# Performance work log

Measured on AMD Instinct MI355X. Metric: run time of the kernel, lower is better.

The kernel has to match this reference:

```python
import jax, jax.numpy as jnp
import numpy as np

D = 256        # node/edge feature dim
H = 256        # MLP hidden dim
NG = 80000     # grid (src) nodes
NM = 20000     # mesh (dst) nodes
E = 160000     # g2m edges
EPS = 1e-5


def _mlp(x, W1, b1, W2, b2, g, beta):
    # MeshGraphMLP with hidden_layers=1: Linear -> SiLU -> Linear -> LayerNorm
    h = jax.nn.silu(x @ W1 + b1)
    y = h @ W2 + b2
    mu = jnp.mean(y, axis=-1, keepdims=True)
    var = jnp.var(y, axis=-1, keepdims=True)
    return (y - mu) * jax.lax.rsqrt(var + EPS) * g + beta


def setup_inputs() -> dict:
    key = jax.random.key(0)
    ks = jax.random.split(key, 16)

    def rn(k, shape, s=0.02):
        return jax.random.normal(k, shape, dtype=jnp.float32) * s

    inp = {
        "g2m_efeat": jax.random.normal(ks[0], (E, D), dtype=jnp.float32),
        "grid_nfeat": jax.random.normal(ks[1], (NG, D), dtype=jnp.float32),
        "mesh_nfeat": jax.random.normal(ks[2], (NM, D), dtype=jnp.float32),
        "src_idx": jax.random.randint(ks[3], (E,), 0, NG, dtype=jnp.int32),
        "dst_idx": jax.random.randint(ks[4], (E,), 0, NM, dtype=jnp.int32),
        # edge MLP (concat variant): input = [efeat | src_feat | dst_feat] -> 3D
        "eW1": rn(ks[5], (3 * D, H)), "eb1": jnp.zeros((H,), jnp.float32),
        "eW2": rn(ks[6], (H, D)),     "eb2": jnp.zeros((D,), jnp.float32),
        "eg": jnp.ones((D,), jnp.float32), "ebeta": jnp.zeros((D,), jnp.float32),
        # src node MLP: D -> H -> D
        "sW1": rn(ks[7], (D, H)), "sb1": jnp.zeros((H,), jnp.float32),
        "sW2": rn(ks[8], (H, D)), "sb2": jnp.zeros((D,), jnp.float32),
        "sg": jnp.ones((D,), jnp.float32), "sbeta": jnp.zeros((D,), jnp.float32),
        # dst node MLP: (D_agg + D_node) = 2D -> H -> D
        "dW1": rn(ks[9], (2 * D, H)), "db1": jnp.zeros((H,), jnp.float32),
        "dW2": rn(ks[10], (H, D)),    "db2": jnp.zeros((D,), jnp.float32),
        "dg": jnp.ones((D,), jnp.float32), "dbeta": jnp.zeros((D,), jnp.float32),
    }
    return inp


def reference(g2m_efeat, grid_nfeat, mesh_nfeat, src_idx, dst_idx,
              eW1, eb1, eW2, eb2, eg, ebeta,
              sW1, sb1, sW2, sb2, sg, sbeta,
              dW1, db1, dW2, db2, dg, dbeta):
    # edge MLP: gather src/dst node features, concat with edge features
    e_in = jnp.concatenate(
        [g2m_efeat, grid_nfeat[src_idx], mesh_nfeat[dst_idx]], axis=-1)  # [E, 3D]
    efeat = _mlp(e_in, eW1, eb1, eW2, eb2, eg, ebeta)                    # [E, D]
    # aggregate_and_concat: copy_e_sum scatter to dst mesh nodes, concat node feats
    agg = jax.ops.segment_sum(efeat, dst_idx, num_segments=NM)           # [NM, D]
    cat_feat = jnp.concatenate([agg, mesh_nfeat], axis=-1)               # [NM, 2D]
    mesh_out = mesh_nfeat + _mlp(cat_feat, dW1, db1, dW2, db2, dg, dbeta)
    grid_out = grid_nfeat + _mlp(grid_nfeat, sW1, sb1, sW2, sb2, sg, sbeta)
    return (grid_out, mesh_out)
```

## Files before the change

kernel.cpp:

```cpp
#include <hip/hip_runtime.h>
#include <hip/hip_bf16.h>

#define DD 256
#define NGN 80000
#define NMN 20000
#define NEE 160000

typedef unsigned short u16;
typedef __attribute__((ext_vector_type(8))) short s16x8;
typedef __attribute__((ext_vector_type(4))) short s16x4;
typedef __attribute__((ext_vector_type(4))) float f32x4;

__device__ __forceinline__ u16 f2bf(float f) {
  union { float f; unsigned u; } v; v.f = f;
  unsigned r = (v.u + 0x7FFFu + ((v.u >> 16) & 1u)) >> 16;
  return (u16)r;
}
__device__ __forceinline__ float bf2f(u16 x) {
  union { unsigned u; float f; } v; v.u = ((unsigned)x) << 16;
  return v.f;
}

__global__ void pack_weights(const float* __restrict__ W, u16* __restrict__ dst, int K) {
  int idx = blockIdx.x * 256 + threadIdx.x;
  if (idx >= K * 256) return;
  int i = idx & 7;
  int lane = (idx >> 3) & 63;
  int nt = (idx >> 9) & 15;
  int kt = idx >> 13;
  int k = kt * 32 + 4 * (lane >> 4) + (i < 4 ? i : 12 + i);
  int n = nt * 16 + (lane & 15);
  dst[idx] = f2bf(W[(size_t)k * 256 + n]);
}

__global__ void csr_hist(const int* __restrict__ didx, int* __restrict__ cnt) {
  int i = blockIdx.x * 256 + threadIdx.x;
  if (i < NEE) atomicAdd(cnt + didx[i], 1);
}
__global__ void csr_scan(const int* __restrict__ cnt, int* __restrict__ cursor) {
  __shared__ int psum[256];
  const int CH = (NMN + 255) / 256;
  int t = threadIdx.x;
  int base = t * CH, s = 0;
  for (int k = 0; k < CH; ++k) { int i = base + k; if (i < NMN) s += cnt[i]; }
  psum[t] = s;
  __syncthreads();
  for (int off = 1; off < 256; off <<= 1) {
    int v = (t >= off) ? psum[t - off] : 0;
    __syncthreads();
    psum[t] += v;
    __syncthreads();
  }
  int run = psum[t] - s;
  for (int k = 0; k < CH; ++k) {
    int i = base + k;
    if (i < NMN) { cursor[i] = run; run += cnt[i]; }
  }
}
__global__ void csr_fill(const int* __restrict__ didx, int* __restrict__ cursor,
                         int* __restrict__ eids) {
  int e = blockIdx.x * 256 + threadIdx.x;
  if (e < NEE) { int p = atomicAdd(cursor + didx[e], 1); eids[p] = e; }
}

__device__ __forceinline__ s16x8 ldsA(const u16* uni, int rowL, int cL) {
  int swz = (rowL & 7) << 4;
  s16x4 lo = *(const s16x4*)((const char*)uni + rowL * 512 + ((cL * 2) ^ swz));
  s16x4 hi = *(const s16x4*)((const char*)uni + rowL * 512 + (((cL + 16) * 2) ^ swz));
  s16x8 a;
#pragma unroll
  for (int j = 0; j < 4; ++j) { a[j] = lo[j]; a[4 + j] = hi[j]; }
  return a;
}

__global__ __launch_bounds__(256, 2) void gemm_ns(
    const float* __restrict__ X, const u16* __restrict__ Wp,
    u16* __restrict__ Y, int n) {
  __shared__ u16 uni[16384];
  const int tid = threadIdx.x;
  const int lane = tid & 63;
  const int wave = tid >> 6;
  const int mr = wave >> 1, nc = wave & 1;
  const int g = lane >> 4, lr = lane & 15;
  const int row0 = blockIdx.x * 64;

#pragma unroll
  for (int j = 0; j < 8; ++j) {
    int e = wave * 16 + j * 2 + (lane >> 5);
    int r = min(row0 + e, n - 1);
    const float* src = X + (size_t)r * DD + (lane & 31) * 8;
    f32x4 f0 = *(const f32x4*)src;
    f32x4 f1 = *(const f32x4*)(src + 4);
    s16x8 o;
#pragma unroll
    for (int k = 0; k < 4; ++k) { o[k] = (short)f2bf(f0[k]); o[4 + k] = (short)f2bf(f1[k]); }
    int co = (lane & 31) * 8;
    *(s16x8*)((char*)uni + e * 512 + ((co * 2) ^ ((e & 7) << 4))) = o;
  }
  __syncthreads();

  const f32x4 fz = {0.f, 0.f, 0.f, 0.f};
  f32x4 acc[2][8];
#pragma unroll
  for (int mt = 0; mt < 2; ++mt)
#pragma unroll
    for (int nt = 0; nt < 8; ++nt) acc[mt][nt] = fz;

  for (int kl = 0; kl < 8; ++kl) {
    s16x8 afr[2];
#pragma unroll
    for (int mt = 0; mt < 2; ++mt) afr[mt] = ldsA(uni, mr * 32 + mt * 16 + lr, kl * 32 + 4 * g);
#pragma unroll
    for (int h = 0; h < 2; ++h) {
      s16x8 bfr[4];
#pragma unroll
      for (int q = 0; q < 4; ++q)
        bfr[q] = *(const s16x8*)(Wp + (size_t)kl * 8192 + ((nc * 8 + h * 4 + q) * 64 + lane) * 8);
#pragma unroll
      for (int q = 0; q < 4; ++q) {
        acc[0][h * 4 + q] = __builtin_amdgcn_mfma_f32_16x16x32_bf16(afr[0], bfr[q], acc[0][h * 4 + q], 0, 0, 0);
        acc[1][h * 4 + q] = __builtin_amdgcn_mfma_f32_16x16x32_bf16(afr[1], bfr[q], acc[1][h * 4 + q], 0, 0, 0);
      }
    }
  }
  __syncthreads();
#pragma unroll
  for (int mt = 0; mt < 2; ++mt)
#pragma unroll
    for (int nt = 0; nt < 8; ++nt)
#pragma unroll
      for (int i = 0; i < 4; ++i) {
        int rowL = mr * 32 + mt * 16 + 4 * g + i;
        int col = nc * 128 + nt * 16 + lr;
        *(u16*)((char*)uni + rowL * 512 + ((col * 2) ^ ((rowL & 7) << 4))) = f2bf(acc[mt][nt][i]);
      }
  __syncthreads();
#pragma unroll
  for (int rr = 0; rr < 16; ++rr) {
    int rowL = wave * 16 + rr;
    int rg = row0 + rowL;
    if (rg < n) {
      s16x4 v = *(const s16x4*)((char*)uni + rowL * 512 + ((lane * 8) ^ ((rowL & 7) << 4)));
      *(s16x4*)(Y + (size_t)rg * DD + lane * 4) = v;
    }
  }
}

__global__ __launch_bounds__(256, 2) void edge_fused(
    const float* __restrict__ efeat,
    const u16* __restrict__ GSp, const u16* __restrict__ GMp,
    const int* __restrict__ sidx, const int* __restrict__ eids,
    const u16* __restrict__ W1p, const float* __restrict__ b1,
    const u16* __restrict__ W2p, const float* __restrict__ b2,
    const float* __restrict__ gam, const float* __restrict__ bet,
    const int* __restrict__ didx, float* __restrict__ agg) {
  __shared__ u16 uni[16384];
  __shared__ float2 pstats[64][2];
  __shared__ int eidL[64];
  __shared__ int srcL[64];
  __shared__ int dstL[64];

  const int tid = threadIdx.x;
  const int lane = tid & 63;
  const int wave = tid >> 6;
  const int mr = wave >> 1, nc = wave & 1;
  const int g = lane >> 4, lr = lane & 15;
  const int row0 = blockIdx.x * 64;

  if (tid < 64) {
    int e = eids[row0 + tid];
    eidL[tid] = e;
    srcL[tid] = sidx[e];
    dstL[tid] = didx[e];
  }
  __syncthreads();

#pragma unroll
  for (int j = 0; j < 8; ++j) {
    int e = wave * 16 + j * 2 + (lane >> 5);
    int co = (lane & 31) * 8;
    s16x8 a = *(const s16x8*)(GSp + (size_t)srcL[e] * DD + co);
    s16x8 b = *(const s16x8*)(GMp + (size_t)dstL[e] * DD + co);
    s16x8 o;
#pragma unroll
    for (int k = 0; k < 8; ++k) o[k] = (short)f2bf(bf2f((u16)a[k]) + bf2f((u16)b[k]));
    *(s16x8*)((char*)uni + e * 512 + ((co * 2) ^ ((e & 7) << 4))) = o;
  }
  __syncthreads();

  f32x4 acc[2][8];
#pragma unroll
  for (int mt = 0; mt < 2; ++mt)
#pragma unroll
    for (int nt = 0; nt < 8; ++nt)
#pragma unroll
      for (int i = 0; i < 4; ++i) {
        int rowL = mr * 32 + mt * 16 + 4 * g + i;
        int col = nc * 128 + nt * 16 + lr;
        acc[mt][nt][i] = bf2f(*(const u16*)((char*)uni + rowL * 512 + ((col * 2) ^ ((rowL & 7) << 4))));
      }
  __syncthreads();

#pragma unroll
  for (int j = 0; j < 8; ++j) {
    int e = wave * 16 + j * 2 + (lane >> 5);
    const float* src = efeat + (size_t)eidL[e] * DD + (lane & 31) * 8;
    f32x4 f0 = *(const f32x4*)src;
    f32x4 f1 = *(const f32x4*)(src + 4);
    s16x8 o;
#pragma unroll
    for (int k = 0; k < 4; ++k) { o[k] = (short)f2bf(f0[k]); o[4 + k] = (short)f2bf(f1[k]); }
    int co = (lane & 31) * 8;
    *(s16x8*)((char*)uni + e * 512 + ((co * 2) ^ ((e & 7) << 4))) = o;
  }
  __syncthreads();

  for (int kl = 0; kl < 8; ++kl) {
    s16x8 afr[2];
#pragma unroll
    for (int mt = 0; mt < 2; ++mt) afr[mt] = ldsA(uni, mr * 32 + mt * 16 + lr, kl * 32 + 4 * g);
#pragma unroll
    for (int h = 0; h < 2; ++h) {
      s16x8 bfr[4];
#pragma unroll
      for (int q = 0; q < 4; ++q)
        bfr[q] = *(const s16x8*)(W1p + (size_t)kl * 8192 + ((nc * 8 + h * 4 + q) * 64 + lane) * 8);
#pragma unroll
      for (int q = 0; q < 4; ++q) {
        acc[0][h * 4 + q] = __builtin_amdgcn_mfma_f32_16x16x32_bf16(afr[0], bfr[q], acc[0][h * 4 + q], 0, 0, 0);
        acc[1][h * 4 + q] = __builtin_amdgcn_mfma_f32_16x16x32_bf16(afr[1], bfr[q], acc[1][h * 4 + q], 0, 0, 0);
      }
    }
  }
  __syncthreads();

  {
    float b1v[8];
#pragma unroll
    for (int nt = 0; nt < 8; ++nt) b1v[nt] = b1[nc * 128 + nt * 16 + lr];
#pragma unroll
    for (int mt = 0; mt < 2; ++mt)
#pragma unroll
      for (int nt = 0; nt < 8; ++nt)
#pragma unroll
        for (int i = 0; i < 4; ++i) {
          float x = acc[mt][nt][i] + b1v[nt];
          float h = x / (1.f + __expf(-x));
          int rowL = mr * 32 + mt * 16 + 4 * g + i;
          int col = nc * 128 + nt * 16 + lr;
          *(u16*)((char*)uni + rowL * 512 + ((col * 2) ^ ((rowL & 7) << 4))) = f2bf(h);
        }
  }
  __syncthreads();

  f32x4 acc2[2][8];
  const f32x4 fz = {0.f, 0.f, 0.f, 0.f};
#pragma unroll
  for (int mt = 0; mt < 2; ++mt)
#pragma unroll
    for (int nt = 0; nt < 8; ++nt) acc2[mt][nt] = fz;
  for (int kl = 0; kl < 8; ++kl) {
    s16x8 afr[2];
#pragma unroll
    for (int mt = 0; mt < 2; ++mt) afr[mt] = ldsA(uni, mr * 32 + mt * 16 + lr, kl * 32 + 4 * g);
#pragma unroll
    for (int h = 0; h < 2; ++h) {
      s16x8 bfr[4];
#pragma unroll
      for (int q = 0; q < 4; ++q)
        bfr[q] = *(const s16x8*)(W2p + (size_t)kl * 8192 + ((nc * 8 + h * 4 + q) * 64 + lane) * 8);
#pragma unroll
      for (int q = 0; q < 4; ++q) {
        acc2[0][h * 4 + q] = __builtin_amdgcn_mfma_f32_16x16x32_bf16(afr[0], bfr[q], acc2[0][h * 4 + q], 0, 0, 0);
        acc2[1][h * 4 + q] = __builtin_amdgcn_mfma_f32_16x16x32_bf16(afr[1], bfr[q], acc2[1][h * 4 + q], 0, 0, 0);
      }
    }
  }

  float b2v[8], gv[8], bv[8];
#pragma unroll
  for (int nt = 0; nt < 8; ++nt) {
    int col = nc * 128 + nt * 16 + lr;
    b2v[nt] = b2[col];
    gv[nt] = gam[col];
    bv[nt] = bet[col];
  }
#pragma unroll
  for (int mt = 0; mt < 2; ++mt)
#pragma unroll
    for (int i = 0; i < 4; ++i) {
      float s = 0.f, s2 = 0.f;
#pragma unroll
      for (int nt = 0; nt < 8; ++nt) {
        float y = acc2[mt][nt][i] + b2v[nt];
        s += y;
        s2 += y * y;
      }
#pragma unroll
      for (int m = 1; m < 16; m <<= 1) {
        s += __shfl_xor(s, m);
        s2 += __shfl_xor(s2, m);
      }
      if (lr == 0) pstats[mr * 32 + mt * 16 + 4 * g + i][nc] = make_float2(s, s2);
    }
  __syncthreads();

#pragma unroll
  for (int mt = 0; mt < 2; ++mt)
#pragma unroll
    for (int i = 0; i < 4; ++i) {
      int rowL = mr * 32 + mt * 16 + 4 * g + i;
      float2 pa = pstats[rowL][0], pb = pstats[rowL][1];
      float sum = pa.x + pb.x, sq = pa.y + pb.y;
      float mu = sum * (1.f / 256.f);
      float var = fmaxf(sq * (1.f / 256.f) - mu * mu, 0.f);
      float rs = rsqrtf(var + 1e-5f);
#pragma unroll
      for (int nt = 0; nt < 8; ++nt) {
        int col = nc * 128 + nt * 16 + lr;
        float y = acc2[mt][nt][i] + b2v[nt];
        float val = (y - mu) * rs * gv[nt] + bv[nt];
        *(u16*)((char*)uni + rowL * 512 + ((col * 2) ^ ((rowL & 7) << 4))) = f2bf(val);
      }
    }
  __syncthreads();

  {
    int c = tid;
    float sum = 0.f;
    int prev = dstL[0];
#pragma unroll 8
    for (int r = 0; r < 64; ++r) {
      int d = dstL[r];
      if (d != prev) {
        atomicAdd(agg + (size_t)prev * DD + c, sum);
        sum = 0.f;
        prev = d;
      }
      sum += bf2f(*(const u16*)((char*)uni + r * 512 + ((c * 2) ^ ((r & 7) << 4))));
    }
    atomicAdd(agg + (size_t)prev * DD + c, sum);
  }
}

template <int MODE, int K1>
__global__ __launch_bounds__(256, 2) void mlp_fused(
    const float* __restrict__ xa, const float* __restrict__ xb,
    const u16* __restrict__ W1p, const float* __restrict__ b1,
    const u16* __restrict__ W2p, const float* __restrict__ b2,
    const float* __restrict__ gam, const float* __restrict__ bet,
    const float* __restrict__ resid, float* __restrict__ out, int nrows) {
  __shared__ u16 uni[16384];
  __shared__ float2 pstats[64][2];

  const int tid = threadIdx.x;
  const int lane = tid & 63;
  const int wave = tid >> 6;
  const int mr = wave >> 1, nc = wave & 1;
  const int g = lane >> 4, lr = lane & 15;
  const int row0 = blockIdx.x * 64;

  const f32x4 fz = {0.f, 0.f, 0.f, 0.f};
  f32x4 acc[2][8];
#pragma unroll
  for (int mt = 0; mt < 2; ++mt)
#pragma unroll
    for (int nt = 0; nt < 8; ++nt) acc[mt][nt] = fz;

#pragma unroll
  for (int region = 0; region < K1 / 256; ++region) {
    __syncthreads();
    const float* Xr = (region == 0) ? xa : xb;
#pragma unroll
    for (int j = 0; j < 8; ++j) {
      int e = wave * 16 + j * 2 + (lane >> 5);
      int r = min(row0 + e, nrows - 1);
      const float* src = Xr + (size_t)r * DD + (lane & 31) * 8;
      f32x4 f0 = *(const f32x4*)src;
      f32x4 f1 = *(const f32x4*)(src + 4);
      s16x8 o;
#pragma unroll
      for (int k = 0; k < 4; ++k) { o[k] = (short)f2bf(f0[k]); o[4 + k] = (short)f2bf(f1[k]); }
      int co = (lane & 31) * 8;
      *(s16x8*)((char*)uni + e * 512 + ((co * 2) ^ ((e & 7) << 4))) = o;
    }
    __syncthreads();
    for (int kl = 0; kl < 8; ++kl) {
      const int kt = region * 8 + kl;
      s16x8 afr[2];
#pragma unroll
      for (int mt = 0; mt < 2; ++mt) afr[mt] = ldsA(uni, mr * 32 + mt * 16 + lr, kl * 32 + 4 * g);
#pragma unroll
      for (int h = 0; h < 2; ++h) {
        s16x8 bfr[4];
#pragma unroll
        for (int q = 0; q < 4; ++q)
          bfr[q] = *(const s16x8*)(W1p + (size_t)kt * 8192 + ((nc * 8 + h * 4 + q) * 64 + lane) * 8);
#pragma unroll
        for (int q = 0; q < 4; ++q) {
          acc[0][h * 4 + q] = __builtin_amdgcn_mfma_f32_16x16x32_bf16(afr[0], bfr[q], acc[0][h * 4 + q], 0, 0, 0);
          acc[1][h * 4 + q] = __builtin_amdgcn_mfma_f32_16x16x32_bf16(afr[1], bfr[q], acc[1][h * 4 + q], 0, 0, 0);
        }
      }
    }
  }
  __syncthreads();

  {
    float b1v[8];
#pragma unroll
    for (int nt = 0; nt < 8; ++nt) b1v[nt] = b1[nc * 128 + nt * 16 + lr];
#pragma unroll
    for (int mt = 0; mt < 2; ++mt)
#pragma unroll
      for (int nt = 0; nt < 8; ++nt)
#pragma unroll
        for (int i = 0; i < 4; ++i) {
          float x = acc[mt][nt][i] + b1v[nt];
          float h = x / (1.f + __expf(-x));
          int rowL = mr * 32 + mt * 16 + 4 * g + i;
          int col = nc * 128 + nt * 16 + lr;
          *(u16*)((char*)uni + rowL * 512 + ((col * 2) ^ ((rowL & 7) << 4))) = f2bf(h);
        }
  }
  __syncthreads();

  f32x4 acc2[2][8];
#pragma unroll
  for (int mt = 0; mt < 2; ++mt)
#pragma unroll
    for (int nt = 0; nt < 8; ++nt) acc2[mt][nt] = fz;
  for (int kl = 0; kl < 8; ++kl) {
    s16x8 afr[2];
#pragma unroll
    for (int mt = 0; mt < 2; ++mt) afr[mt] = ldsA(uni, mr * 32 + mt * 16 + lr, kl * 32 + 4 * g);
#pragma unroll
    for (int h = 0; h < 2; ++h) {
      s16x8 bfr[4];
#pragma unroll
      for (int q = 0; q < 4; ++q)
        bfr[q] = *(const s16x8*)(W2p + (size_t)kl * 8192 + ((nc * 8 + h * 4 + q) * 64 + lane) * 8);
#pragma unroll
      for (int q = 0; q < 4; ++q) {
        acc2[0][h * 4 + q] = __builtin_amdgcn_mfma_f32_16x16x32_bf16(afr[0], bfr[q], acc2[0][h * 4 + q], 0, 0, 0);
        acc2[1][h * 4 + q] = __builtin_amdgcn_mfma_f32_16x16x32_bf16(afr[1], bfr[q], acc2[1][h * 4 + q], 0, 0, 0);
      }
    }
  }

  float b2v[8], gv[8], bv[8];
#pragma unroll
  for (int nt = 0; nt < 8; ++nt) {
    int col = nc * 128 + nt * 16 + lr;
    b2v[nt] = b2[col];
    gv[nt] = gam[col];
    bv[nt] = bet[col];
  }
#pragma unroll
  for (int mt = 0; mt < 2; ++mt)
#pragma unroll
    for (int i = 0; i < 4; ++i) {
      float s = 0.f, s2 = 0.f;
#pragma unroll
      for (int nt = 0; nt < 8; ++nt) {
        float y = acc2[mt][nt][i] + b2v[nt];
        s += y;
        s2 += y * y;
      }
#pragma unroll
      for (int m = 1; m < 16; m <<= 1) {
        s += __shfl_xor(s, m);
        s2 += __shfl_xor(s2, m);
      }
      if (lr == 0) pstats[mr * 32 + mt * 16 + 4 * g + i][nc] = make_float2(s, s2);
    }
  __syncthreads();
#pragma unroll
  for (int mt = 0; mt < 2; ++mt)
#pragma unroll
    for (int i = 0; i < 4; ++i) {
      int rowL = mr * 32 + mt * 16 + 4 * g + i;
      float2 pa = pstats[rowL][0], pb = pstats[rowL][1];
      float sum = pa.x + pb.x, sq = pa.y + pb.y;
      float mu = sum * (1.f / 256.f);
      float var = fmaxf(sq * (1.f / 256.f) - mu * mu, 0.f);
      float rs = rsqrtf(var + 1e-5f);
      int rg = row0 + rowL;
      if (MODE == 2 && rg >= nrows) continue;
#pragma unroll
      for (int nt = 0; nt < 8; ++nt) {
        int col = nc * 128 + nt * 16 + lr;
        float y = acc2[mt][nt][i] + b2v[nt];
        float val = (y - mu) * rs * gv[nt] + bv[nt];
        out[(size_t)rg * DD + col] = resid[(size_t)rg * DD + col] + val;
      }
    }
}

extern "C" void kernel_launch(void* const* d_in, const int* in_sizes, int n_in,
                              void* d_out, int out_size, void* d_ws, size_t ws_size,
                              hipStream_t stream) {
  const float* g2m  = (const float*)d_in[0];
  const float* grid = (const float*)d_in[1];
  const float* mesh = (const float*)d_in[2];
  const int* sidx = (const int*)d_in[3];
  const int* didx = (const int*)d_in[4];
  const float* eW1 = (const float*)d_in[5];
  const float* eb1 = (const float*)d_in[6];
  const float* eW2 = (const float*)d_in[7];
  const float* eb2 = (const float*)d_in[8];
  const float* eg  = (const float*)d_in[9];
  const float* ebt = (const float*)d_in[10];
  const float* sW1 = (const float*)d_in[11];
  const float* sb1 = (const float*)d_in[12];
  const float* sW2 = (const float*)d_in[13];
  const float* sb2 = (const float*)d_in[14];
  const float* sg  = (const float*)d_in[15];
  const float* sbt = (const float*)d_in[16];
  const float* dW1 = (const float*)d_in[17];
  const float* db1 = (const float*)d_in[18];
  const float* dW2 = (const float*)d_in[19];
  const float* db2 = (const float*)d_in[20];
  const float* dg  = (const float*)d_in[21];
  const float* dbt = (const float*)d_in[22];

  char* w = (char*)d_ws;
  float* agg = (float*)w;
  u16* wp = (u16*)(w + 20480000);
  int* cnt = (int*)(w + 20480000 + 1179648);
  int* cursor = cnt + 20480;
  int* eids = cursor + 20480;

  u16* eW1p = wp;
  u16* eW2p = eW1p + 768 * 256;
  u16* sW1p = eW2p + 256 * 256;
  u16* sW2p = sW1p + 256 * 256;
  u16* dW1p = sW2p + 256 * 256;
  u16* dW2p = dW1p + 512 * 256;

  float* gout = (float*)d_out;
  float* mout = gout + (size_t)NGN * DD;
  u16* GSp = (u16*)d_out;
  u16* GMp = GSp + (size_t)NGN * DD;

  (void)hipMemsetAsync(agg, 0, 20480000, stream);
  (void)hipMemsetAsync(cnt, 0, 81920, stream);

  pack_weights<<<768, 256, 0, stream>>>(eW1, eW1p, 768);
  pack_weights<<<256, 256, 0, stream>>>(eW2, eW2p, 256);
  pack_weights<<<256, 256, 0, stream>>>(sW1, sW1p, 256);
  pack_weights<<<256, 256, 0, stream>>>(sW2, sW2p, 256);
  pack_weights<<<512, 256, 0, stream>>>(dW1, dW1p, 512);
  pack_weights<<<256, 256, 0, stream>>>(dW2, dW2p, 256);

  csr_hist<<<(NEE + 255) / 256, 256, 0, stream>>>(didx, cnt);
  csr_scan<<<1, 256, 0, stream>>>(cnt, cursor);
  csr_fill<<<(NEE + 255) / 256, 256, 0, stream>>>(didx, cursor, eids);

  gemm_ns<<<NGN / 64, 256, 0, stream>>>(grid, eW1p + 8 * 8192, GSp, NGN);
  gemm_ns<<<(NMN + 63) / 64, 256, 0, stream>>>(mesh, eW1p + 16 * 8192, GMp, NMN);

  edge_fused<<<NEE / 64, 256, 0, stream>>>(
      g2m, GSp, GMp, sidx, eids, eW1p, eb1, eW2p, eb2, eg, ebt, didx, agg);

  mlp_fused<2, 512><<<(NMN + 63) / 64, 256, 0, stream>>>(
      agg, mesh, dW1p, db1, dW2p, db2, dg, dbt, mesh, mout, NMN);
  mlp_fused<1, 256><<<NGN / 64, 256, 0, stream>>>(
      grid, nullptr, sW1p, sb1, sW2p, sb2, sg, sbt, grid, gout, NGN);
}
```

Baseline: 426.0 us.

## Merge small launches and co-schedule grid MLP blocks with edge MLP blocks

Folds the six weight-pack launches and the CSR histogram into one kernel, and merges the projection GEMMs with the CSR fill into another. When workspace allows, the projected node features move out of the output buffer so the grid-node MLP can run interleaved with edge blocks (every third block) in one launch, removing the serial dependency. The goal is fewer launches and better overlap of independent work. The cost is larger kernels whose branch-dependent register and shared-memory use may lower occupancy. Rounding now goes through the library bf16 conversion.

```diff
diff --git a/kernel.cpp b/kernel.cpp
--- a/kernel.cpp
+++ b/kernel.cpp
@@ -12,31 +12,50 @@
 typedef __attribute__((ext_vector_type(4))) float f32x4;
 
 __device__ __forceinline__ u16 f2bf(float f) {
-  union { float f; unsigned u; } v; v.f = f;
-  unsigned r = (v.u + 0x7FFFu + ((v.u >> 16) & 1u)) >> 16;
-  return (u16)r;
+  __hip_bfloat16 h = __float2bfloat16(f);
+  union { __hip_bfloat16 h; u16 u; } v; v.h = h;
+  return v.u;
 }
 __device__ __forceinline__ float bf2f(u16 x) {
   union { unsigned u; float f; } v; v.u = ((unsigned)x) << 16;
   return v.f;
 }
 
-__global__ void pack_weights(const float* __restrict__ W, u16* __restrict__ dst, int K) {
-  int idx = blockIdx.x * 256 + threadIdx.x;
-  if (idx >= K * 256) return;
-  int i = idx & 7;
-  int lane = (idx >> 3) & 63;
-  int nt = (idx >> 9) & 15;
-  int kt = idx >> 13;
-  int k = kt * 32 + 4 * (lane >> 4) + (i < 4 ? i : 12 + i);
-  int n = nt * 16 + (lane & 15);
-  dst[idx] = f2bf(W[(size_t)k * 256 + n]);
-}
-
-__global__ void csr_hist(const int* __restrict__ didx, int* __restrict__ cnt) {
-  int i = blockIdx.x * 256 + threadIdx.x;
-  if (i < NEE) atomicAdd(cnt + didx[i], 1);
-}
+__device__ __forceinline__ s16x8 ldsA(const u16* uni, int rowL, int cL) {
+  int swz = (rowL & 7) << 4;
+  s16x4 lo = *(const s16x4*)((const char*)uni + rowL * 512 + ((cL * 2) ^ swz));
+  s16x4 hi = *(const s16x4*)((const char*)uni + rowL * 512 + (((cL + 16) * 2) ^ swz));
+  s16x8 a;
+#pragma unroll
+  for (int j = 0; j < 4; ++j) { a[j] = lo[j]; a[4 + j] = hi[j]; }
+  return a;
+}
+
+__global__ void pack_hist(const float* __restrict__ eW1, const float* __restrict__ eW2,
+                          const float* __restrict__ sW1, const float* __restrict__ sW2,
+                          const float* __restrict__ dW1, const float* __restrict__ dW2,
+                          u16* __restrict__ wp, const int* __restrict__ didx,
+                          int* __restrict__ cnt) {
+  int bid = blockIdx.x;
+  if (bid < 2304) {
+    const float* W; u16* dst; int lb;
+    if (bid < 768)       { W = eW1; dst = wp;              lb = bid; }
+    else if (bid < 1024) { W = eW2; dst = wp + 768 * 256;  lb = bid - 768; }
+    else if (bid < 1280) { W = sW1; dst = wp + 1024 * 256; lb = bid - 1024; }
+    else if (bid < 1536) { W = sW2; dst = wp + 1280 * 256; lb = bid - 1280; }
+    else if (bid < 2048) { W = dW1; dst = wp + 1536 * 256; lb = bid - 1536; }
+    else                 { W = dW2; dst = wp + 2048 * 256; lb = bid - 2048; }
+    int idx = lb * 256 + threadIdx.x;
+    int i = idx & 7, lane = (idx >> 3) & 63, nt = (idx >> 9) & 15, kt = idx >> 13;
+    int k = kt * 32 + 4 * (lane >> 4) + (i < 4 ? i : 12 + i);
+    int n = nt * 16 + (lane & 15);
+    dst[idx] = f2bf(W[(size_t)k * 256 + n]);
+  } else {
+    int i = (bid - 2304) * 256 + threadIdx.x;
+    if (i < NEE) atomicAdd(cnt + didx[i], 1);
+  }
+}
+
 __global__ void csr_scan(const int* __restrict__ cnt, int* __restrict__ cursor) {
   __shared__ int psum[256];
   const int CH = (NMN + 255) / 256;
@@ -57,32 +76,16 @@
     if (i < NMN) { cursor[i] = run; run += cnt[i]; }
   }
 }
-__global__ void csr_fill(const int* __restrict__ didx, int* __restrict__ cursor,
-                         int* __restrict__ eids) {
-  int e = blockIdx.x * 256 + threadIdx.x;
-  if (e < NEE) { int p = atomicAdd(cursor + didx[e], 1); eids[p] = e; }
-}
-
-__device__ __forceinline__ s16x8 ldsA(const u16* uni, int rowL, int cL) {
-  int swz = (rowL & 7) << 4;
-  s16x4 lo = *(const s16x4*)((const char*)uni + rowL * 512 + ((cL * 2) ^ swz));
-  s16x4 hi = *(const s16x4*)((const char*)uni + rowL * 512 + (((cL + 16) * 2) ^ swz));
-  s16x8 a;
-#pragma unroll
-  for (int j = 0; j < 4; ++j) { a[j] = lo[j]; a[4 + j] = hi[j]; }
-  return a;
-}
-
-__global__ __launch_bounds__(256, 2) void gemm_ns(
-    const float* __restrict__ X, const u16* __restrict__ Wp,
-    u16* __restrict__ Y, int n) {
-  __shared__ u16 uni[16384];
+
+__device__ __forceinline__ void gemm_body(u16* uni, const float* __restrict__ X,
+                                          const u16* __restrict__ Wp, u16* __restrict__ Y,
+                                          int n, int blk) {
   const int tid = threadIdx.x;
   const int lane = tid & 63;
   const int wave = tid >> 6;
   const int mr = wave >> 1, nc = wave & 1;
   const int g = lane >> 4, lr = lane & 15;
-  const int row0 = blockIdx.x * 64;
+  const int row0 = blk * 64;
 
 #pragma unroll
   for (int j = 0; j < 8; ++j) {
@@ -146,26 +149,187 @@
   }
 }
 
-__global__ __launch_bounds__(256, 2) void edge_fused(
+__global__ __launch_bounds__(256, 2) void gemm_fill(
+    const float* __restrict__ gridf, const float* __restrict__ mesh,
+    const u16* __restrict__ wp, u16* __restrict__ GSp, u16* __restrict__ GMp,
+    const int* __restrict__ didx, int* __restrict__ cursor, int* __restrict__ eids) {
+  __shared__ u16 uni[16384];
+  int bid = blockIdx.x;
+  if (bid < 1250) gemm_body(uni, gridf, wp + 8 * 8192, GSp, NGN, bid);
+  else if (bid < 1563) gemm_body(uni, mesh, wp + 16 * 8192, GMp, NMN, bid - 1250);
+  else {
+    int e = (bid - 1563) * 256 + threadIdx.x;
+    if (e < NEE) { int p = atomicAdd(cursor + didx[e], 1); eids[p] = e; }
+  }
+}
+
+template <int MODE, int K1>
+__device__ __forceinline__ void mlp_body(
+    u16* uni, float2 (*pstats)[2],
+    const float* __restrict__ xa, const float* __restrict__ xb,
+    const u16* __restrict__ W1p, const float* __restrict__ b1,
+    const u16* __restrict__ W2p, const float* __restrict__ b2,
+    const float* __restrict__ gam, const float* __restrict__ bet,
+    const float* __restrict__ resid, float* __restrict__ out, int nrows, int blk) {
+  const int tid = threadIdx.x;
+  const int lane = tid & 63;
+  const int wave = tid >> 6;
+  const int mr = wave >> 1, nc = wave & 1;
+  const int g = lane >> 4, lr = lane & 15;
+  const int row0 = blk * 64;
+
+  const f32x4 fz = {0.f, 0.f, 0.f, 0.f};
+  f32x4 acc[2][8];
+#pragma unroll
+  for (int mt = 0; mt < 2; ++mt)
+#pragma unroll
+    for (int nt = 0; nt < 8; ++nt) acc[mt][nt] = fz;
+
+#pragma unroll
+  for (int region = 0; region < K1 / 256; ++region) {
+    __syncthreads();
+    const float* Xr = (region == 0) ? xa : xb;
+#pragma unroll
+    for (int j = 0; j < 8; ++j) {
+      int e = wave * 16 + j * 2 + (lane >> 5);
+      int r = min(row0 + e, nrows - 1);
+      const float* src = Xr + (size_t)r * DD + (lane & 31) * 8;
+      f32x4 f0 = *(const f32x4*)src;
+      f32x4 f1 = *(const f32x4*)(src + 4);
+      s16x8 o;
+#pragma unroll
+      for (int k = 0; k < 4; ++k) { o[k] = (short)f2bf(f0[k]); o[4 + k] = (short)f2bf(f1[k]); }
+      int co = (lane & 31) * 8;
+      *(s16x8*)((char*)uni + e * 512 + ((co * 2) ^ ((e & 7) << 4))) = o;
+    }
+    __syncthreads();
+    for (int kl = 0; kl < 8; ++kl) {
+      const int kt = region * 8 + kl;
+      s16x8 afr[2];
+#pragma unroll
+      for (int mt = 0; mt < 2; ++mt) afr[mt] = ldsA(uni, mr * 32 + mt * 16 + lr, kl * 32 + 4 * g);
+#pragma unroll
+      for (int h = 0; h < 2; ++h) {
+        s16x8 bfr[4];
+#pragma unroll
+        for (int q = 0; q < 4; ++q)
+          bfr[q] = *(const s16x8*)(W1p + (size_t)kt * 8192 + ((nc * 8 + h * 4 + q) * 64 + lane) * 8);
+#pragma unroll
+        for (int q = 0; q < 4; ++q) {
+          acc[0][h * 4 + q] = __builtin_amdgcn_mfma_f32_16x16x32_bf16(afr[0], bfr[q], acc[0][h * 4 + q], 0, 0, 0);
+          acc[1][h * 4 + q] = __builtin_amdgcn_mfma_f32_16x16x32_bf16(afr[1], bfr[q], acc[1][h * 4 + q], 0, 0, 0);
+        }
+      }
+    }
+  }
+  __syncthreads();
+
+  {
+    float b1v[8];
+#pragma unroll
+    for (int nt = 0; nt < 8; ++nt) b1v[nt] = b1[nc * 128 + nt * 16 + lr];
+#pragma unroll
+    for (int mt = 0; mt < 2; ++mt)
+#pragma unroll
+      for (int nt = 0; nt < 8; ++nt)
+#pragma unroll
+        for (int i = 0; i < 4; ++i) {
+          float x = acc[mt][nt][i] + b1v[nt];
+          float h = x / (1.f + __expf(-x));
+          int rowL = mr * 32 + mt * 16 + 4 * g + i;
+          int col = nc * 128 + nt * 16 + lr;
+          *(u16*)((char*)uni + rowL * 512 + ((col * 2) ^ ((rowL & 7) << 4))) = f2bf(h);
+        }
+  }
+  __syncthreads();
+
+  f32x4 acc2[2][8];
+#pragma unroll
+  for (int mt = 0; mt < 2; ++mt)
+#pragma unroll
+    for (int nt = 0; nt < 8; ++nt) acc2[mt][nt] = fz;
+  for (int kl = 0; kl < 8; ++kl) {
+    s16x8 afr[2];
+#pragma unroll
+    for (int mt = 0; mt < 2; ++mt) afr[mt] = ldsA(uni, mr * 32 + mt * 16 + lr, kl * 32 + 4 * g);
+#pragma unroll
+    for (int h = 0; h < 2; ++h) {
+      s16x8 bfr[4];
+#pragma unroll
+      for (int q = 0; q < 4; ++q)
+        bfr[q] = *(const s16x8*)(W2p + (size_t)kl * 8192 + ((nc * 8 + h * 4 + q) * 64 + lane) * 8);
+#pragma unroll
+      for (int q = 0; q < 4; ++q) {
+        acc2[0][h * 4 + q] = __builtin_amdgcn_mfma_f32_16x16x32_bf16(afr[0], bfr[q], acc2[0][h * 4 + q], 0, 0, 0);
+        acc2[1][h * 4 + q] = __builtin_amdgcn_mfma_f32_16x16x32_bf16(afr[1], bfr[q], acc2[1][h * 4 + q], 0, 0, 0);
+      }
+    }
+  }
+
+  float b2v[8], gv[8], bv[8];
+#pragma unroll
+  for (int nt = 0; nt < 8; ++nt) {
+    int col = nc * 128 + nt * 16 + lr;
+    b2v[nt] = b2[col];
+    gv[nt] = gam[col];
+    bv[nt] = bet[col];
+  }
+#pragma unroll
+  for (int mt = 0; mt < 2; ++mt)
+#pragma unroll
+    for (int i = 0; i < 4; ++i) {
+      float s = 0.f, s2 = 0.f;
+#pragma unroll
+      for (int nt = 0; nt < 8; ++nt) {
+        float y = acc2[mt][nt][i] + b2v[nt];
+        s += y;
+        s2 += y * y;
+      }
+#pragma unroll
+      for (int m = 1; m < 16; m <<= 1) {
+        s += __shfl_xor(s, m);
+        s2 += __shfl_xor(s2, m);
+      }
+      if (lr == 0) pstats[mr * 32 + mt * 16 + 4 * g + i][nc] = make_float2(s, s2);
+    }
+  __syncthreads();
+#pragma unroll
+  for (int mt = 0; mt < 2; ++mt)
+#pragma unroll
+    for (int i = 0; i < 4; ++i) {
+      int rowL = mr * 32 + mt * 16 + 4 * g + i;
+      float2 pa = pstats[rowL][0], pb = pstats[rowL][1];
+      float sum = pa.x + pb.x, sq = pa.y + pb.y;
+      float mu = sum * (1.f / 256.f);
+      float var = fmaxf(sq * (1.f / 256.f) - mu * mu, 0.f);
+      float rs = rsqrtf(var + 1e-5f);
+      int rg = row0 + rowL;
+      if (MODE == 2 && rg >= nrows) continue;
+#pragma unroll
+      for (int nt = 0; nt < 8; ++nt) {
+        int col = nc * 128 + nt * 16 + lr;
+        float y = acc2[mt][nt][i] + b2v[nt];
+        float val = (y - mu) * rs * gv[nt] + bv[nt];
+        out[(size_t)rg * DD + col] = resid[(size_t)rg * DD + col] + val;
+      }
+    }
+}
+
+__device__ __forceinline__ void edge_body(
+    u16* uni, float2 (*pstats)[2], int* eidL, int* srcL, int* dstL,
     const float* __restrict__ efeat,
     const u16* __restrict__ GSp, const u16* __restrict__ GMp,
     const int* __restrict__ sidx, const int* __restrict__ eids,
     const u16* __restrict__ W1p, const float* __restrict__ b1,
     const u16* __restrict__ W2p, const float* __restrict__ b2,
     const float* __restrict__ gam, const float* __restrict__ bet,
-    const int* __restrict__ didx, float* __restrict__ agg) {
-  __shared__ u16 uni[16384];
-  __shared__ float2 pstats[64][2];
-  __shared__ int eidL[64];
-  __shared__ int srcL[64];
-  __shared__ int dstL[64];
-
+    const int* __restrict__ didx, float* __restrict__ agg, int blk) {
   const int tid = threadIdx.x;
   const int lane = tid & 63;
   const int wave = tid >> 6;
   const int mr = wave >> 1, nc = wave & 1;
   const int g = lane >> 4, lr = lane & 15;
-  const int row0 = blockIdx.x * 64;
+  const int row0 = blk * 64;
 
   if (tid < 64) {
     int e = eids[row0 + tid];
@@ -183,7 +347,8 @@
     s16x8 b = *(const s16x8*)(GMp + (size_t)dstL[e] * DD + co);
     s16x8 o;
 #pragma unroll
-    for (int k = 0; k < 8; ++k) o[k] = (short)f2bf(bf2f((u16)a[k]) + bf2f((u16)b[k]));
+    for (int k2 = 0; k2 < 8; ++k2)
+      o[k2] = (short)f2bf(bf2f((u16)a[k2]) + bf2f((u16)b[k2]));
     *(s16x8*)((char*)uni + e * 512 + ((co * 2) ^ ((e & 7) << 4))) = o;
   }
   __syncthreads();
@@ -343,158 +508,57 @@
   }
 }
 
-template <int MODE, int K1>
-__global__ __launch_bounds__(256, 2) void mlp_fused(
-    const float* __restrict__ xa, const float* __restrict__ xb,
+__global__ __launch_bounds__(256, 2) void edge_mlp(
+    const float* __restrict__ efeat,
+    const u16* __restrict__ GSp, const u16* __restrict__ GMp,
+    const int* __restrict__ sidx, const int* __restrict__ eids,
+    const u16* __restrict__ eW1p, const float* __restrict__ eb1,
+    const u16* __restrict__ eW2p, const float* __restrict__ eb2,
+    const float* __restrict__ eg, const float* __restrict__ ebt,
+    const int* __restrict__ didx, float* __restrict__ agg,
+    const float* __restrict__ gridf,
+    const u16* __restrict__ sW1p, const float* __restrict__ sb1,
+    const u16* __restrict__ sW2p, const float* __restrict__ sb2,
+    const float* __restrict__ sg, const float* __restrict__ sbt,
+    float* __restrict__ gout, int withMlp) {
+  __shared__ u16 uni[16384];
+  __shared__ float2 pstats[64][2];
+  __shared__ int eidL[64], srcL[64], dstL[64];
+  int bid = blockIdx.x;
+  if (withMlp) {
+    if ((bid % 3) == 2) {
+      mlp_body<1, 256>(uni, pstats, gridf, nullptr, sW1p, sb1, sW2p, sb2,
+                       sg, sbt, gridf, gout, NGN, bid / 3);
+      return;
+    }
+    bid = (bid / 3) * 2 + (bid % 3);
+  }
+  edge_body(uni, pstats, eidL, srcL, dstL, efeat, GSp, GMp, sidx, eids,
+            eW1p, eb1, eW2p, eb2, eg, ebt, didx, agg, bid);
+}
+
+__global__ __launch_bounds__(256, 2) void mlp1_kernel(
+    const float* __restrict__ gridf,
     const u16* __restrict__ W1p, const float* __restrict__ b1,
     const u16* __restrict__ W2p, const float* __restrict__ b2,
     const float* __restrict__ gam, const float* __restrict__ bet,
-    const float* __restrict__ resid, float* __restrict__ out, int nrows) {
+    float* __restrict__ out) {
   __shared__ u16 uni[16384];
   __shared__ float2 pstats[64][2];
-
-  const int tid = threadIdx.x;
-  const int lane = tid & 63;
-  const int wave = tid >> 6;
-  const int mr = wave >> 1, nc = wave & 1;
-  const int g = lane >> 4, lr = lane & 15;
-  const int row0 = blockIdx.x * 64;
-
-  const f32x4 fz = {0.f, 0.f, 0.f, 0.f};
-  f32x4 acc[2][8];
-#pragma unroll
-  for (int mt = 0; mt < 2; ++mt)
-#pragma unroll
-    for (int nt = 0; nt < 8; ++nt) acc[mt][nt] = fz;
-
-#pragma unroll
-  for (int region = 0; region < K1 / 256; ++region) {
-    __syncthreads();
-    const float* Xr = (region == 0) ? xa : xb;
-#pragma unroll
-    for (int j = 0; j < 8; ++j) {
-      int e = wave * 16 + j * 2 + (lane >> 5);
-      int r = min(row0 + e, nrows - 1);
-      const float* src = Xr + (size_t)r * DD + (lane & 31) * 8;
-      f32x4 f0 = *(const f32x4*)src;
-      f32x4 f1 = *(const f32x4*)(src + 4);
-      s16x8 o;
-#pragma unroll
-      for (int k = 0; k < 4; ++k) { o[k] = (short)f2bf(f0[k]); o[4 + k] = (short)f2bf(f1[k]); }
-      int co = (lane & 31) * 8;
-      *(s16x8*)((char*)uni + e * 512 + ((co * 2) ^ ((e & 7) << 4))) = o;
-    }
-    __syncthreads();
-    for (int kl = 0; kl < 8; ++kl) {
-      const int kt = region * 8 + kl;
-      s16x8 afr[2];
-#pragma unroll
-      for (int mt = 0; mt < 2; ++mt) afr[mt] = ldsA(uni, mr * 32 + mt * 16 + lr, kl * 32 + 4 * g);
-#pragma unroll
-      for (int h = 0; h < 2; ++h) {
-        s16x8 bfr[4];
-#pragma unroll
-        for (int q = 0; q < 4; ++q)
-          bfr[q] = *(const s16x8*)(W1p + (size_t)kt * 8192 + ((nc * 8 + h * 4 + q) * 64 + lane) * 8);
-#pragma unroll
-        for (int q = 0; q < 4; ++q) {
-          acc[0][h * 4 + q] = __builtin_amdgcn_mfma_f32_16x16x32_bf16(afr[0], bfr[q], acc[0][h * 4 + q], 0, 0, 0);
-          acc[1][h * 4 + q] = __builtin_amdgcn_mfma_f32_16x16x32_bf16(afr[1], bfr[q], acc[1][h * 4 + q], 0, 0, 0);
-        }
-      }
-    }
-  }
-  __syncthreads();
-
-  {
-    float b1v[8];
-#pragma unroll
-    for (int nt = 0; nt < 8; ++nt) b1v[nt] = b1[nc * 128 + nt * 16 + lr];
-#pragma unroll
-    for (int mt = 0; mt < 2; ++mt)
-#pragma unroll
-      for (int nt = 0; nt < 8; ++nt)
-#pragma unroll
-        for (int i = 0; i < 4; ++i) {
-          float x = acc[mt][nt][i] + b1v[nt];
-          float h = x / (1.f + __expf(-x));
-          int rowL = mr * 32 + mt * 16 + 4 * g + i;
-          int col = nc * 128 + nt * 16 + lr;
-          *(u16*)((char*)uni + rowL * 512 + ((col * 2) ^ ((rowL & 7) << 4))) = f2bf(h);
-        }
-  }
-  __syncthreads();
-
-  f32x4 acc2[2][8];
-#pragma unroll
-  for (int mt = 0; mt < 2; ++mt)
-#pragma unroll
-    for (int nt = 0; nt < 8; ++nt) acc2[mt][nt] = fz;
-  for (int kl = 0; kl < 8; ++kl) {
-    s16x8 afr[2];
-#pragma unroll
-    for (int mt = 0; mt < 2; ++mt) afr[mt] = ldsA(uni, mr * 32 + mt * 16 + lr, kl * 32 + 4 * g);
-#pragma unroll
-    for (int h = 0; h < 2; ++h) {
-      s16x8 bfr[4];
-#pragma unroll
-      for (int q = 0; q < 4; ++q)
-        bfr[q] = *(const s16x8*)(W2p + (size_t)kl * 8192 + ((nc * 8 + h * 4 + q) * 64 + lane) * 8);
-#pragma unroll
-      for (int q = 0; q < 4; ++q) {
-        acc2[0][h * 4 + q] = __builtin_amdgcn_mfma_f32_16x16x32_bf16(afr[0], bfr[q], acc2[0][h * 4 + q], 0, 0, 0);
-        acc2[1][h * 4 + q] = __builtin_amdgcn_mfma_f32_16x16x32_bf16(afr[1], bfr[q], acc2[1][h * 4 + q], 0, 0, 0);
-      }
-    }
-  }
-
-  float b2v[8], gv[8], bv[8];
-#pragma unroll
-  for (int nt = 0; nt < 8; ++nt) {
-    int col = nc * 128 + nt * 16 + lr;
-    b2v[nt] = b2[col];
-    gv[nt] = gam[col];
-    bv[nt] = bet[col];
-  }
-#pragma unroll
-  for (int mt = 0; mt < 2; ++mt)
-#pragma unroll
-    for (int i = 0; i < 4; ++i) {
-      float s = 0.f, s2 = 0.f;
-#pragma unroll
-      for (int nt = 0; nt < 8; ++nt) {
-        float y = acc2[mt][nt][i] + b2v[nt];
-        s += y;
-        s2 += y * y;
-      }
-#pragma unroll
-      for (int m = 1; m < 16; m <<= 1) {
-        s += __shfl_xor(s, m);
-        s2 += __shfl_xor(s2, m);
-      }
-      if (lr == 0) pstats[mr * 32 + mt * 16 + 4 * g + i][nc] = make_float2(s, s2);
-    }
-  __syncthreads();
-#pragma unroll
-  for (int mt = 0; mt < 2; ++mt)
-#pragma unroll
-    for (int i = 0; i < 4; ++i) {
-      int rowL = mr * 32 + mt * 16 + 4 * g + i;
-      float2 pa = pstats[rowL][0], pb = pstats[rowL][1];
-      float sum = pa.x + pb.x, sq = pa.y + pb.y;
-      float mu = sum * (1.f / 256.f);
-      float var = fmaxf(sq * (1.f / 256.f) - mu * mu, 0.f);
-      float rs = rsqrtf(var + 1e-5f);
-      int rg = row0 + rowL;
-      if (MODE == 2 && rg >= nrows) continue;
-#pragma unroll
-      for (int nt = 0; nt < 8; ++nt) {
-        int col = nc * 128 + nt * 16 + lr;
-        float y = acc2[mt][nt][i] + b2v[nt];
-        float val = (y - mu) * rs * gv[nt] + bv[nt];
-        out[(size_t)rg * DD + col] = resid[(size_t)rg * DD + col] + val;
-      }
-    }
+  mlp_body<1, 256>(uni, pstats, gridf, nullptr, W1p, b1, W2p, b2, gam, bet,
+                   gridf, out, NGN, blockIdx.x);
+}
+
+__global__ __launch_bounds__(256, 2) void mlp2_kernel(
+    const float* __restrict__ agg, const float* __restrict__ mesh,
+    const u16* __restrict__ W1p, const float* __restrict__ b1,
+    const u16* __restrict__ W2p, const float* __restrict__ b2,
+    const float* __restrict__ gam, const float* __restrict__ bet,
+    float* __restrict__ out) {
+  __shared__ u16 uni[16384];
+  __shared__ float2 pstats[64][2];
+  mlp_body<2, 512>(uni, pstats, agg, mesh, W1p, b1, W2p, b2, gam, bet,
+                   mesh, out, NMN, blockIdx.x);
 }
 
 extern "C" void kernel_launch(void* const* d_in, const int* in_sizes, int n_in,
@@ -530,6 +594,8 @@
   int* cnt = (int*)(w + 20480000 + 1179648);
   int* cursor = cnt + 20480;
   int* eids = cursor + 20480;
+  const size_t GS_OFF = 22463488;
+  const size_t NEEDED = GS_OFF + (size_t)NGN * DD * 2 + (size_t)NMN * DD * 2;
 
   u16* eW1p = wp;
   u16* eW2p = eW1p + 768 * 256;
@@ -540,31 +606,31 @@
 
   float* gout = (float*)d_out;
   float* mout = gout + (size_t)NGN * DD;
-  u16* GSp = (u16*)d_out;
+
+  const bool big = ws_size >= NEEDED;
+  u16* GSp = big ? (u16*)(w + GS_OFF) : (u16*)d_out;
   u16* GMp = GSp + (size_t)NGN * DD;
 
   (void)hipMemsetAsync(agg, 0, 20480000, stream);
   (void)hipMemsetAsync(cnt, 0, 81920, stream);
 
-  pack_weights<<<768, 256, 0, stream>>>(eW1, eW1p, 768);
-  pack_weights<<<256, 256, 0, stream>>>(eW2, eW2p, 256);
-  pack_weights<<<256, 256, 0, stream>>>(sW1, sW1p, 256);
-  pack_weights<<<256, 256, 0, stream>>>(sW2, sW2p, 256);
-  pack_weights<<<512, 256, 0, stream>>>(dW1, dW1p, 512);
-  pack_weights<<<256, 256, 0, stream>>>(dW2, dW2p, 256);
-
-  csr_hist<<<(NEE + 255) / 256, 256, 0, stream>>>(didx, cnt);
+  pack_hist<<<2304 + 625, 256, 0, stream>>>(eW1, eW2, sW1, sW2, dW1, dW2, wp, didx, cnt);
   csr_scan<<<1, 256, 0, stream>>>(cnt, cursor);
-  csr_fill<<<(NEE + 255) / 256, 256, 0, stream>>>(didx, cursor, eids);
-
-  gemm_ns<<<NGN / 64, 256, 0, stream>>>(grid, eW1p + 8 * 8192, GSp, NGN);
-  gemm_ns<<<(NMN + 63) / 64, 256, 0, stream>>>(mesh, eW1p + 16 * 8192, GMp, NMN);
-
-  edge_fused<<<NEE / 64, 256, 0, stream>>>(
-      g2m, GSp, GMp, sidx, eids, eW1p, eb1, eW2p, eb2, eg, ebt, didx, agg);
-
-  mlp_fused<2, 512><<<(NMN + 63) / 64, 256, 0, stream>>>(
-      agg, mesh, dW1p, db1, dW2p, db2, dg, dbt, mesh, mout, NMN);
-  mlp_fused<1, 256><<<NGN / 64, 256, 0, stream>>>(
-      grid, nullptr, sW1p, sb1, sW2p, sb2, sg, sbt, grid, gout, NGN);
-}
+  gemm_fill<<<1563 + 625, 256, 0, stream>>>(grid, mesh, wp, GSp, GMp, didx, cursor, eids);
+
+  if (big) {
+    edge_mlp<<<3750, 256, 0, stream>>>(
+        g2m, GSp, GMp, sidx, eids, eW1p, eb1, eW2p, eb2, eg, ebt, didx, agg,
+        grid, sW1p, sb1, sW2p, sb2, sg, sbt, gout, 1);
+    mlp2_kernel<<<(NMN + 63) / 64, 256, 0, stream>>>(
+        agg, mesh, dW1p, db1, dW2p, db2, dg, dbt, mout);
+  } else {
+    edge_mlp<<<2500, 256, 0, stream>>>(
+        g2m, GSp, GMp, sidx, eids, eW1p, eb1, eW2p, eb2, eg, ebt, didx, agg,
+        grid, sW1p, sb1, sW2p, sb2, sg, sbt, gout, 0);
+    mlp2_kernel<<<(NMN + 63) / 64, 256, 0, stream>>>(
+        agg, mesh, dW1p, db1, dW2p, db2, dg, dbt, mout);
+    mlp1_kernel<<<NGN / 64, 256, 0, stream>>>(
+        grid, sW1p, sb1, sW2p, sb2, sg, sbt, gout);
+  }
+}
```

New measurement: 360.6 us. 1.18x faster.
